# Optimization experiments

Hardware: AMD Instinct MI355X
Metric: run time of the kernel (lower is better)

The kernel has to match this reference:

```python
import jax, jax.numpy as jnp
import numpy as np

N_SRC = 200000
N_TGT = 40000
NNZ = 280000
D_IN = 256
D_OUT = 256
LN_EPS = 1e-5


def setup_inputs() -> dict:
    key = jax.random.key(0)
    ks = jax.random.split(key, 6)
    x = jax.random.normal(ks[0], (N_SRC, D_IN), dtype=jnp.float32)
    rows = jax.random.randint(ks[1], (NNZ,), 0, N_TGT, dtype=jnp.int32)
    cols = jax.random.randint(ks[2], (NNZ,), 0, N_SRC, dtype=jnp.int32)
    vals = jax.random.uniform(ks[3], (NNZ,), dtype=jnp.float32)
    # Linear(in_dim, out_dim) params (PyTorch-style init scale)
    W = jax.random.normal(ks[4], (D_IN, D_OUT), dtype=jnp.float32) / np.sqrt(D_IN)
    b = jnp.zeros((D_OUT,), dtype=jnp.float32)
    # LayerNorm(out_dim) params
    gamma = jnp.ones((D_OUT,), dtype=jnp.float32)
    beta = jnp.zeros((D_OUT,), dtype=jnp.float32)
    return {"x": x, "rows": rows, "cols": cols, "vals": vals,
            "W": W, "b": b, "gamma": gamma, "beta": beta,
            "num_targets": N_TGT}


def reference(x, rows, cols, vals, W, b, gamma, beta, num_targets):
    # SpMM: mapped[t, :] = sum_{e: rows[e]==t} vals[e] * x[cols[e], :]
    contrib = x[cols] * vals[:, None]                      # [nnz, d_in]
    mapped = jax.ops.segment_sum(contrib, rows, num_segments=num_targets)  # [n_tgt, d_in]
    # Linear
    h = mapped @ W + b                                     # [n_tgt, d_out]
    # LayerNorm
    mu = jnp.mean(h, axis=-1, keepdims=True)
    var = jnp.mean(jnp.square(h - mu), axis=-1, keepdims=True)
    normed = (h - mu) * jax.lax.rsqrt(var + LN_EPS) * gamma + beta
    # GELU (exact erf form, matches torch nn.GELU default)
    return jax.nn.gelu(normed, approximate=False)
```

## Files before the change

### kernel.cpp

```cpp
#include <hip/hip_runtime.h>
#include <math.h>

#define D 256
#define TM 32
#define KC 8
#define LN_EPS 1e-5f
#define SCAN_CHUNK 1024

__global__ __launch_bounds__(256) void hist_kernel(
    const int* __restrict__ rows, int* __restrict__ cnt, int nnz)
{
    const int e = blockIdx.x * 256 + threadIdx.x;
    if (e < nnz) atomicAdd(&cnt[rows[e]], 1);
}

__global__ __launch_bounds__(256) void scan1_kernel(
    const int* __restrict__ cnt, int* __restrict__ row_ptr,
    int* __restrict__ partials, int n)
{
    const int tid = threadIdx.x;
    const int base = blockIdx.x * SCAN_CHUNK + tid * 4;
    int v[4];
#pragma unroll
    for (int q = 0; q < 4; q++) {
        const int i = base + q;
        v[q] = (i < n) ? cnt[i] : 0;
    }
    const int tsum = v[0] + v[1] + v[2] + v[3];

    const int lane = tid & 63;
    int s = tsum;
#pragma unroll
    for (int off = 1; off < 64; off <<= 1) {
        const int t = __shfl_up(s, off);
        if (lane >= off) s += t;
    }
    __shared__ int wtot[4];
    if (lane == 63) wtot[tid >> 6] = s;
    __syncthreads();
    const int w = tid >> 6;
    int woff = 0;
#pragma unroll
    for (int u = 0; u < 4; u++) if (u < w) woff += wtot[u];

    int run = woff + s - tsum;
#pragma unroll
    for (int q = 0; q < 4; q++) {
        const int i = base + q;
        if (i < n) row_ptr[i] = run;
        run += v[q];
    }
    if (tid == 255) partials[blockIdx.x] = woff + s;
}

__global__ __launch_bounds__(256) void scan23_kernel(
    int* __restrict__ row_ptr, int* __restrict__ cursor,
    const int* __restrict__ partials, int n, int nnz, int nb)
{
    const int tid = threadIdx.x;
    __shared__ int s_add;
    if (tid < 64) {
        const int v = (tid < nb) ? partials[tid] : 0;
        int s = v;
#pragma unroll
        for (int off = 1; off < 64; off <<= 1) {
            const int u = __shfl_up(s, off);
            if (tid >= off) s += u;
        }
        if (tid == (int)blockIdx.x) s_add = s - v;
    }
    __syncthreads();
    const int add = s_add;

    const int base = blockIdx.x * SCAN_CHUNK + tid * 4;
#pragma unroll
    for (int q = 0; q < 4; q++) {
        const int i = base + q;
        if (i < n) {
            const int rp = row_ptr[i] + add;
            row_ptr[i] = rp;
            cursor[i]  = rp;
        }
    }
    if (blockIdx.x == 0 && tid == 0) row_ptr[n] = nnz;
}

__global__ __launch_bounds__(256) void reorder_kernel(
    const int* __restrict__ rows, const int* __restrict__ cols,
    const float* __restrict__ vals, int* __restrict__ cursor,
    int* __restrict__ scol, float* __restrict__ sval, int nnz)
{
    const int e = blockIdx.x * 256 + threadIdx.x;
    if (e < nnz) {
        const int r = rows[e];
        const int pos = atomicAdd(&cursor[r], 1);
        scol[pos] = cols[e];
        sval[pos] = vals[e];
    }
}

__global__ __launch_bounds__(256, 4) void fused_spmm_gemm_kernel(
    const float* __restrict__ x, const int* __restrict__ row_ptr,
    const int* __restrict__ scol, const float* __restrict__ sval,
    const float* __restrict__ Wm, const float* __restrict__ bias,
    const float* __restrict__ gamma, const float* __restrict__ beta,
    float* __restrict__ out)
{
    __shared__ float As[TM][D];
    __shared__ float Bs[KC][D];

    const int tid  = threadIdx.x;
    const int wv   = tid >> 6;
    const int lane = tid & 63;
    const int r0   = blockIdx.x * TM;

    const int rbase = r0 + wv * 8;
    int rp = 0;
    if (lane < 9) rp = row_ptr[rbase + lane];
    const int rbeg = __shfl(rp, 0);
    const int rend = __shfl(rp, 8);

    int wbase = rbeg;
    int   cidx = 0;
    float cval = 0.f;
    {
        const int tot = min(64, rend - wbase);
        if (lane < tot) {
            cidx = scol[wbase + lane];
            cval = sval[wbase + lane];
        }
    }

    for (int rr = 0; rr < 8; rr++) {
        const int beg = __shfl(rp, rr);
        const int end = __shfl(rp, rr + 1);

        float4 a0 = make_float4(0.f, 0.f, 0.f, 0.f);
        float4 a1 = a0, a2 = a0, a3 = a0;

        int e = beg;
        while (e < end) {
            if (e >= wbase + 64) {
                wbase = e;
                const int tot = min(64, rend - wbase);
                cidx = (lane < tot) ? scol[wbase + lane] : 0;
                cval = (lane < tot) ? sval[wbase + lane] : 0.f;
            }
            const int avail = min(end - e, wbase + 64 - e);
            const int bcnt  = min(8, avail);

            int   cc[8];
            float vv[8];
#pragma unroll
            for (int u = 0; u < 8; u++) {
                const int sl = (u < bcnt) ? (e + u - wbase) : (e - wbase);
                cc[u] = __shfl(cidx, sl);
                const float fv = __shfl(cval, sl);
                vv[u] = (u < bcnt) ? fv : 0.f;
            }

            const float* p0 = x + (size_t)cc[0] * D + 4 * lane;
            const float* p1 = x + (size_t)cc[1] * D + 4 * lane;
            const float* p2 = x + (size_t)cc[2] * D + 4 * lane;
            const float* p3 = x + (size_t)cc[3] * D + 4 * lane;
            const float* p4 = x + (size_t)cc[4] * D + 4 * lane;
            const float* p5 = x + (size_t)cc[5] * D + 4 * lane;
            const float* p6 = x + (size_t)cc[6] * D + 4 * lane;
            const float* p7 = x + (size_t)cc[7] * D + 4 * lane;
            float4 x0, x1, x2, x3, x4, x5, x6, x7;
#define GLD(dst, ptr) \
    asm volatile("global_load_dwordx4 %0, %1, off" : "=v"(dst) : "v"(ptr))
            GLD(x0, p0); GLD(x1, p1); GLD(x2, p2); GLD(x3, p3);
            GLD(x4, p4); GLD(x5, p5); GLD(x6, p6); GLD(x7, p7);
#undef GLD
            asm volatile("s_waitcnt vmcnt(0)" ::: "memory");
            __builtin_amdgcn_sched_barrier(0);

            a0.x = fmaf(vv[0], x0.x, a0.x); a0.y = fmaf(vv[0], x0.y, a0.y);
            a0.z = fmaf(vv[0], x0.z, a0.z); a0.w = fmaf(vv[0], x0.w, a0.w);
            a1.x = fmaf(vv[1], x1.x, a1.x); a1.y = fmaf(vv[1], x1.y, a1.y);
            a1.z = fmaf(vv[1], x1.z, a1.z); a1.w = fmaf(vv[1], x1.w, a1.w);
            a2.x = fmaf(vv[2], x2.x, a2.x); a2.y = fmaf(vv[2], x2.y, a2.y);
            a2.z = fmaf(vv[2], x2.z, a2.z); a2.w = fmaf(vv[2], x2.w, a2.w);
            a3.x = fmaf(vv[3], x3.x, a3.x); a3.y = fmaf(vv[3], x3.y, a3.y);
            a3.z = fmaf(vv[3], x3.z, a3.z); a3.w = fmaf(vv[3], x3.w, a3.w);
            a0.x = fmaf(vv[4], x4.x, a0.x); a0.y = fmaf(vv[4], x4.y, a0.y);
            a0.z = fmaf(vv[4], x4.z, a0.z); a0.w = fmaf(vv[4], x4.w, a0.w);
            a1.x = fmaf(vv[5], x5.x, a1.x); a1.y = fmaf(vv[5], x5.y, a1.y);
            a1.z = fmaf(vv[5], x5.z, a1.z); a1.w = fmaf(vv[5], x5.w, a1.w);
            a2.x = fmaf(vv[6], x6.x, a2.x); a2.y = fmaf(vv[6], x6.y, a2.y);
            a2.z = fmaf(vv[6], x6.z, a2.z); a2.w = fmaf(vv[6], x6.w, a2.w);
            a3.x = fmaf(vv[7], x7.x, a3.x); a3.y = fmaf(vv[7], x7.y, a3.y);
            a3.z = fmaf(vv[7], x7.z, a3.z); a3.w = fmaf(vv[7], x7.w, a3.w);

            e += bcnt;
        }
        const float4 s = make_float4(a0.x + a1.x + a2.x + a3.x,
                                     a0.y + a1.y + a2.y + a3.y,
                                     a0.z + a1.z + a2.z + a3.z,
                                     a0.w + a1.w + a2.w + a3.w);
        *(float4*)&As[wv * 8 + rr][4 * lane] = s;
    }
    __syncthreads();

    const int tr = tid >> 5;
    const int tc = tid & 31;

    float acc[4][8];
#pragma unroll
    for (int i = 0; i < 4; i++)
#pragma unroll
        for (int j = 0; j < 8; j++) acc[i][j] = 0.f;

    for (int k0 = 0; k0 < D; k0 += KC) {
#pragma unroll
        for (int q = 0; q < 2; q++) {
            const int idx = q * 256 + tid;
            const int kk = idx >> 6;
            const int c4 = (idx & 63) * 4;
            *(float4*)&Bs[kk][c4] = *(const float4*)(Wm + (size_t)(k0 + kk) * D + c4);
        }
        __syncthreads();

#pragma unroll
        for (int q = 0; q < 2; q++) {
            float4 a4[4];
#pragma unroll
            for (int i = 0; i < 4; i++)
                a4[i] = *(const float4*)&As[tr * 4 + i][k0 + q * 4];
#pragma unroll
            for (int kk = 0; kk < 4; kk++) {
                const float4 b0 = *(const float4*)&Bs[q * 4 + kk][4 * tc];
                const float4 b1 = *(const float4*)&Bs[q * 4 + kk][128 + 4 * tc];
#pragma unroll
                for (int i = 0; i < 4; i++) {
                    const float ai = (kk == 0) ? a4[i].x :
                                     (kk == 1) ? a4[i].y :
                                     (kk == 2) ? a4[i].z : a4[i].w;
                    acc[i][0] = fmaf(ai, b0.x, acc[i][0]);
                    acc[i][1] = fmaf(ai, b0.y, acc[i][1]);
                    acc[i][2] = fmaf(ai, b0.z, acc[i][2]);
                    acc[i][3] = fmaf(ai, b0.w, acc[i][3]);
                    acc[i][4] = fmaf(ai, b1.x, acc[i][4]);
                    acc[i][5] = fmaf(ai, b1.y, acc[i][5]);
                    acc[i][6] = fmaf(ai, b1.z, acc[i][6]);
                    acc[i][7] = fmaf(ai, b1.w, acc[i][7]);
                }
            }
        }
        __syncthreads();
    }

    float gm[8], bt[8], bs[8];
#pragma unroll
    for (int j = 0; j < 8; j++) {
        const int c = (j < 4) ? (4 * tc + j) : (128 + 4 * tc + (j - 4));
        gm[j] = gamma[c]; bt[j] = beta[c]; bs[j] = bias[c];
    }

#pragma unroll
    for (int i = 0; i < 4; i++) {
        float s = 0.f, ss = 0.f;
#pragma unroll
        for (int j = 0; j < 8; j++) {
            const float h = acc[i][j] + bs[j];
            acc[i][j] = h;
            s += h; ss += h * h;
        }
#pragma unroll
        for (int off = 16; off > 0; off >>= 1) {
            s  += __shfl_xor(s,  off);
            ss += __shfl_xor(ss, off);
        }
        const float mean = s * (1.f / D);
        const float var  = ss * (1.f / D) - mean * mean;
        const float rstd = rsqrtf(var + LN_EPS);

        const int row = r0 + tr * 4 + i;
        float y[8];
#pragma unroll
        for (int j = 0; j < 8; j++) {
            const float v = (acc[i][j] - mean) * rstd * gm[j] + bt[j];
            y[j] = 0.5f * v * (1.f + erff(v * 0.70710678118654752f));
        }
        float* op = out + (size_t)row * D;
        *(float4*)(op + 4 * tc)       = make_float4(y[0], y[1], y[2], y[3]);
        *(float4*)(op + 128 + 4 * tc) = make_float4(y[4], y[5], y[6], y[7]);
    }
}

extern "C" void kernel_launch(void* const* d_in, const int* in_sizes, int n_in,
                              void* d_out, int out_size, void* d_ws, size_t ws_size,
                              hipStream_t stream) {
    const float* x     = (const float*)d_in[0];
    const int*   rows  = (const int*)d_in[1];
    const int*   cols  = (const int*)d_in[2];
    const float* vals  = (const float*)d_in[3];
    const float* Wm    = (const float*)d_in[4];
    const float* bias  = (const float*)d_in[5];
    const float* gamma = (const float*)d_in[6];
    const float* beta  = (const float*)d_in[7];
    float* out = (float*)d_out;

    const int nnz   = in_sizes[1];
    const int n_tgt = out_size / D;

    int* cnt      = (int*)d_ws;
    int* row_ptr  = cnt + n_tgt;
    int* cursor   = row_ptr + n_tgt + 1;
    int* partials = cursor + n_tgt;
    int* scol     = partials + 64;
    float* sval   = (float*)(scol + nnz);

    (void)hipMemsetAsync(cnt, 0, (size_t)n_tgt * sizeof(int), stream);

    const int eblocks = (nnz + 255) / 256;
    hist_kernel<<<eblocks, 256, 0, stream>>>(rows, cnt, nnz);

    const int sblocks = (n_tgt + SCAN_CHUNK - 1) / SCAN_CHUNK;
    scan1_kernel<<<sblocks, 256, 0, stream>>>(cnt, row_ptr, partials, n_tgt);
    scan23_kernel<<<sblocks, 256, 0, stream>>>(row_ptr, cursor, partials,
                                               n_tgt, nnz, sblocks);

    reorder_kernel<<<eblocks, 256, 0, stream>>>(rows, cols, vals, cursor,
                                                scol, sval, nnz);

    const int gblocks = n_tgt / TM;
    fused_spmm_gemm_kernel<<<gblocks, 256, 0, stream>>>(
        x, row_ptr, scol, sval, Wm, bias, gamma, beta, out);
}
```

Measured before the change: 420.7 us.

## Make GEMM epilogue wave-local, reading W directly from global

Each wave now computes the linear layer for only the 8 rows it aggregated, reading those rows from its own slice of shared memory. W is streamed from global memory (L2) in float4s instead of being staged through a shared-memory tile. This drops the block-wide barriers and the shared B buffer, and the LayerNorm reduction now runs across the full 64-lane wave. In exchange every wave re-reads all of W from cache, so W global traffic grows roughly fourfold, and each A value is used for 4 output columns rather than 8.

```diff
diff --git a/kernel.cpp b/kernel.cpp
--- a/kernel.cpp
+++ b/kernel.cpp
@@ -3,7 +3,6 @@
 
 #define D 256
 #define TM 32
-#define KC 8
 #define LN_EPS 1e-5f
 #define SCAN_CHUNK 1024
 
@@ -107,7 +106,6 @@
     float* __restrict__ out)
 {
     __shared__ float As[TM][D];
-    __shared__ float Bs[KC][D];
 
     const int tid  = threadIdx.x;
     const int wv   = tid >> 6;
@@ -201,74 +199,63 @@
                                      a0.w + a1.w + a2.w + a3.w);
         *(float4*)&As[wv * 8 + rr][4 * lane] = s;
     }
-    __syncthreads();
-
-    const int tr = tid >> 5;
-    const int tc = tid & 31;
-
-    float acc[4][8];
-#pragma unroll
-    for (int i = 0; i < 4; i++)
-#pragma unroll
-        for (int j = 0; j < 8; j++) acc[i][j] = 0.f;
-
-    for (int k0 = 0; k0 < D; k0 += KC) {
-#pragma unroll
-        for (int q = 0; q < 2; q++) {
-            const int idx = q * 256 + tid;
-            const int kk = idx >> 6;
-            const int c4 = (idx & 63) * 4;
-            *(float4*)&Bs[kk][c4] = *(const float4*)(Wm + (size_t)(k0 + kk) * D + c4);
-        }
-        __syncthreads();
-
-#pragma unroll
-        for (int q = 0; q < 2; q++) {
-            float4 a4[4];
-#pragma unroll
-            for (int i = 0; i < 4; i++)
-                a4[i] = *(const float4*)&As[tr * 4 + i][k0 + q * 4];
-#pragma unroll
-            for (int kk = 0; kk < 4; kk++) {
-                const float4 b0 = *(const float4*)&Bs[q * 4 + kk][4 * tc];
-                const float4 b1 = *(const float4*)&Bs[q * 4 + kk][128 + 4 * tc];
-#pragma unroll
-                for (int i = 0; i < 4; i++) {
-                    const float ai = (kk == 0) ? a4[i].x :
-                                     (kk == 1) ? a4[i].y :
-                                     (kk == 2) ? a4[i].z : a4[i].w;
-                    acc[i][0] = fmaf(ai, b0.x, acc[i][0]);
-                    acc[i][1] = fmaf(ai, b0.y, acc[i][1]);
-                    acc[i][2] = fmaf(ai, b0.z, acc[i][2]);
-                    acc[i][3] = fmaf(ai, b0.w, acc[i][3]);
-                    acc[i][4] = fmaf(ai, b1.x, acc[i][4]);
-                    acc[i][5] = fmaf(ai, b1.y, acc[i][5]);
-                    acc[i][6] = fmaf(ai, b1.z, acc[i][6]);
-                    acc[i][7] = fmaf(ai, b1.w, acc[i][7]);
-                }
-            }
-        }
-        __syncthreads();
-    }
-
-    float gm[8], bt[8], bs[8];
-#pragma unroll
-    for (int j = 0; j < 8; j++) {
-        const int c = (j < 4) ? (4 * tc + j) : (128 + 4 * tc + (j - 4));
+
+    float acc[8][4];
+#pragma unroll
+    for (int r = 0; r < 8; r++)
+#pragma unroll
+        for (int j = 0; j < 4; j++) acc[r][j] = 0.f;
+
+#pragma unroll 2
+    for (int kq = 0; kq < D / 4; kq++) {
+        const int k = kq * 4;
+        const float4 w0 = *(const float4*)(Wm + (size_t)(k + 0) * D + 4 * lane);
+        const float4 w1 = *(const float4*)(Wm + (size_t)(k + 1) * D + 4 * lane);
+        const float4 w2 = *(const float4*)(Wm + (size_t)(k + 2) * D + 4 * lane);
+        const float4 w3 = *(const float4*)(Wm + (size_t)(k + 3) * D + 4 * lane);
+        float4 ar[8];
+#pragma unroll
+        for (int r = 0; r < 8; r++)
+            ar[r] = *(const float4*)&As[wv * 8 + r][k];
+#pragma unroll
+        for (int r = 0; r < 8; r++) {
+            acc[r][0] = fmaf(ar[r].x, w0.x, acc[r][0]);
+            acc[r][1] = fmaf(ar[r].x, w0.y, acc[r][1]);
+            acc[r][2] = fmaf(ar[r].x, w0.z, acc[r][2]);
+            acc[r][3] = fmaf(ar[r].x, w0.w, acc[r][3]);
+            acc[r][0] = fmaf(ar[r].y, w1.x, acc[r][0]);
+            acc[r][1] = fmaf(ar[r].y, w1.y, acc[r][1]);
+            acc[r][2] = fmaf(ar[r].y, w1.z, acc[r][2]);
+            acc[r][3] = fmaf(ar[r].y, w1.w, acc[r][3]);
+            acc[r][0] = fmaf(ar[r].z, w2.x, acc[r][0]);
+            acc[r][1] = fmaf(ar[r].z, w2.y, acc[r][1]);
+            acc[r][2] = fmaf(ar[r].z, w2.z, acc[r][2]);
+            acc[r][3] = fmaf(ar[r].z, w2.w, acc[r][3]);
+            acc[r][0] = fmaf(ar[r].w, w3.x, acc[r][0]);
+            acc[r][1] = fmaf(ar[r].w, w3.y, acc[r][1]);
+            acc[r][2] = fmaf(ar[r].w, w3.z, acc[r][2]);
+            acc[r][3] = fmaf(ar[r].w, w3.w, acc[r][3]);
+        }
+    }
+
+    float gm[4], bt[4], bs[4];
+#pragma unroll
+    for (int j = 0; j < 4; j++) {
+        const int c = 4 * lane + j;
         gm[j] = gamma[c]; bt[j] = beta[c]; bs[j] = bias[c];
     }
 
 #pragma unroll
-    for (int i = 0; i < 4; i++) {
+    for (int rr = 0; rr < 8; rr++) {
+        float h[4];
         float s = 0.f, ss = 0.f;
 #pragma unroll
-        for (int j = 0; j < 8; j++) {
-            const float h = acc[i][j] + bs[j];
-            acc[i][j] = h;
-            s += h; ss += h * h;
-        }
-#pragma unroll
-        for (int off = 16; off > 0; off >>= 1) {
+        for (int j = 0; j < 4; j++) {
+            h[j] = acc[rr][j] + bs[j];
+            s += h[j]; ss += h[j] * h[j];
+        }
+#pragma unroll
+        for (int off = 32; off > 0; off >>= 1) {
             s  += __shfl_xor(s,  off);
             ss += __shfl_xor(ss, off);
         }
@@ -276,16 +263,14 @@
         const float var  = ss * (1.f / D) - mean * mean;
         const float rstd = rsqrtf(var + LN_EPS);
 
-        const int row = r0 + tr * 4 + i;
-        float y[8];
-#pragma unroll
-        for (int j = 0; j < 8; j++) {
-            const float v = (acc[i][j] - mean) * rstd * gm[j] + bt[j];
+        float y[4];
+#pragma unroll
+        for (int j = 0; j < 4; j++) {
+            const float v = (h[j] - mean) * rstd * gm[j] + bt[j];
             y[j] = 0.5f * v * (1.f + erff(v * 0.70710678118654752f));
         }
-        float* op = out + (size_t)row * D;
-        *(float4*)(op + 4 * tc)       = make_float4(y[0], y[1], y[2], y[3]);
-        *(float4*)(op + 128 + 4 * tc) = make_float4(y[4], y[5], y[6], y[7]);
+        float* op = out + (size_t)(rbase + rr) * D;
+        *(float4*)(op + 4 * lane) = make_float4(y[0], y[1], y[2], y[3]);
     }
 }
 
```

Result: slower. 445.4 us (+5.9%).
